# Kernel tuning notes

Measured on AMD Instinct MI355X. Metric: run time of the kernel, lower is better.

Reference implementation:

```python
import jax, jax.numpy as jnp
import numpy as np

B, S, H = 1, 2048, 1024
NH, HD = 16, 64          # num heads, head dim (H = NH*HD)
NT = 1024                # param token num (qkv_slot_num = proj_slot_num)


def pattention(x, key_tokens, value_tokens):
    """Pattention with gelu_l2_norm: x:[...,H] -> [...,out]."""
    attn = jnp.einsum('bsh,th->bst', x, key_tokens)          # scale_factor = 1
    g = jax.nn.gelu(attn, approximate=False)                 # torch F.gelu exact
    norm = jnp.linalg.norm(g, axis=-1, keepdims=True)
    w = g / norm * jnp.sqrt(jnp.asarray(g.shape[-1], g.dtype))
    return jnp.einsum('bst,td->bsd', w, value_tokens)


def setup_inputs() -> dict:
    key = jax.random.key(0)
    ks = jax.random.split(key, 9)
    names = ['q_key', 'q_val', 'k_key', 'k_val', 'v_key', 'v_val', 'proj_key', 'proj_val']
    inp = {'x': jax.random.normal(ks[0], (B, S, H), jnp.float32)}
    for i, n in enumerate(names):
        inp[n] = jax.random.normal(ks[i + 1], (NT, H), jnp.float32) * 0.02
    return inp


def reference(x, q_key, q_val, k_key, k_val, v_key, v_val, proj_key, proj_val):
    # Q/K/V via Pattention (token-parameter attention)
    q = pattention(x, q_key, q_val).reshape(B, S, NH, HD)
    k = pattention(x, k_key, k_val).reshape(B, S, NH, HD)
    v = pattention(x, v_key, v_val).reshape(B, S, NH, HD)
    # causal softmax attention, scale = 1/sqrt(head_dim) (flash default)
    scale = 1.0 / jnp.sqrt(jnp.asarray(HD, q.dtype))
    scores = jnp.einsum('bqhd,bkhd->bhqk', q, k) * scale
    causal = jnp.tril(jnp.ones((S, S), dtype=bool))
    scores = jnp.where(causal, scores, jnp.asarray(-1e30, scores.dtype))
    probs = jax.nn.softmax(scores, axis=-1)
    ctx = jnp.einsum('bhqk,bkhd->bqhd', probs, v).reshape(B, S, H)
    # output projection via Pattention
    return pattention(ctx, proj_key, proj_val)
```

## Files before the change

kernel.cpp:

```cpp
#include <hip/hip_runtime.h>
#include <cstdint>
#include <cstddef>

#define S_LEN 2048
#define H_DIM 1024
#define NTOK  1024
#define NHEAD 16
#define HDIM  64
#define NSPLIT 4

typedef __bf16 bf16;
typedef __bf16 bf16x8 __attribute__((ext_vector_type(8)));
typedef __bf16 bf16x4 __attribute__((ext_vector_type(4)));
typedef float  f32x4  __attribute__((ext_vector_type(4)));

#define QSCALE_LOG2E 0.18033688011112042f

static __device__ __forceinline__ f32x4 mfma16(bf16x8 a, bf16x8 b, f32x4 c) {
    return __builtin_amdgcn_mfma_f32_16x16x32_bf16(a, b, c, 0, 0, 0);
}

static __device__ __forceinline__ void async16(const void* gp, void* lp) {
    __builtin_amdgcn_global_load_lds(
        (const __attribute__((address_space(1))) void*)gp,
        (__attribute__((address_space(3))) void*)lp, 16, 0, 0);
}

static __device__ __forceinline__ float fexp2(float x) {
    return __builtin_amdgcn_exp2f(x);
}

struct PrepArgs {
    const float* csrc[6];
    bf16* cdst[6];
    const float* tsrc[4];
    bf16* tdst[4];
    float* ssq;
};
__global__ __launch_bounds__(256) void prep_kernel(PrepArgs a) {
    __shared__ float t[32][33];
    if (blockIdx.y < 6) {
        if (blockIdx.y == 0 && blockIdx.x == 0) {
#pragma unroll
            for (int i = 0; i < 24; ++i) a.ssq[threadIdx.x + i * 256] = 0.0f;
        }
        const float* __restrict__ s = a.csrc[blockIdx.y];
        bf16* __restrict__ d = a.cdst[blockIdx.y];
        size_t i = ((size_t)blockIdx.x * 256 + threadIdx.x) * 4;
        f32x4 v = *(const f32x4*)&s[i];
        bf16x4 o;
        o[0] = (bf16)v[0]; o[1] = (bf16)v[1]; o[2] = (bf16)v[2]; o[3] = (bf16)v[3];
        *(bf16x4*)&d[i] = o;
    } else {
        const int z = blockIdx.y - 6;
        const float* __restrict__ in = a.tsrc[z];
        bf16* __restrict__ out = a.tdst[z];
        const int bx = (blockIdx.x & 31) * 32, by = (blockIdx.x >> 5) * 32;
        const int x = threadIdx.x & 31, y0 = threadIdx.x >> 5;
#pragma unroll
        for (int j = 0; j < 32; j += 8)
            t[y0 + j][x] = in[(size_t)(by + y0 + j) * 1024 + bx + x];
        __syncthreads();
#pragma unroll
        for (int j = 0; j < 32; j += 8)
            out[(size_t)(bx + y0 + j) * 1024 + by + x] = (bf16)t[x][y0 + j];
    }
}

template <int MODE, typename OutT>
struct GemmArgs {
    const bf16* A[3];
    const bf16* B[3];
    OutT* C[3];
    float* S[3];
    bf16* Ct[3];
    float emul[3];
};

template <int MODE, typename OutT>
__global__ __launch_bounds__(256, 3) void gemm_bt(GemmArgs<MODE, OutT> args) {
    constexpr int Kd = 1024, Nd = 1024, BK = 64;
    const bf16* __restrict__ A = args.A[blockIdx.z];
    const bf16* __restrict__ B = args.B[blockIdx.z];
    OutT* __restrict__ C = args.C[blockIdx.z];
    float* __restrict__ S = args.S[blockIdx.z];
    bf16* __restrict__ Ct = args.Ct[blockIdx.z];
    const float emul = args.emul[blockIdx.z];

    __shared__ __align__(16) bf16 As[2][128 * BK];
    __shared__ __align__(16) bf16 Bs[2][64 * BK];

    const int tid = threadIdx.x;
    const int w = tid >> 6, lane = tid & 63, quad = lane >> 4, m16 = lane & 15;
    const int wm = (w >> 1) * 64, wn = (w & 1) * 32;
    const int bm = blockIdx.y * 128, bn = blockIdx.x * 64;

    const int srow = lane >> 3;
    const int sseg = ((lane & 7) ^ srow) * 8;

    auto stage = [&](int buf, int k0) {
        const bf16* Ab = A + (size_t)bm * Kd + k0;
#pragma unroll
        for (int c = 0; c < 4; ++c) {
            int chunk = w * 4 + c;
            async16(Ab + (size_t)(chunk * 8 + srow) * Kd + sseg,
                    &As[buf][chunk * 512]);
        }
        const bf16* Bb = B + (size_t)bn * Kd + k0;
#pragma unroll
        for (int c = 0; c < 2; ++c) {
            int chunk = w * 2 + c;
            async16(Bb + (size_t)(chunk * 8 + srow) * Kd + sseg,
                    &Bs[buf][chunk * 512]);
        }
    };

    f32x4 acc[4][2] = {};
    stage(0, 0);

    for (int k0 = 0; k0 < Kd; k0 += BK) {
        const int buf = (k0 >> 6) & 1;
        asm volatile("s_waitcnt vmcnt(0)" ::: "memory");
        __syncthreads();
        if (k0 + BK < Kd) stage(buf ^ 1, k0 + BK);

        bf16x8 a[2][4], b[2][2];
#pragma unroll
        for (int kc = 0; kc < 2; ++kc) {
#pragma unroll
            for (int i = 0; i < 4; ++i) {
                int row = wm + i * 16 + m16;
                a[kc][i] = *(const bf16x8*)
                    &As[buf][row * 64 + (((kc * 4 + quad) ^ (row & 7)) << 3)];
            }
#pragma unroll
            for (int j = 0; j < 2; ++j) {
                int row = wn + j * 16 + m16;
                b[kc][j] = *(const bf16x8*)
                    &Bs[buf][row * 64 + (((kc * 4 + quad) ^ (row & 7)) << 3)];
            }
        }
#pragma unroll
        for (int kc = 0; kc < 2; ++kc)
#pragma unroll
            for (int i = 0; i < 4; ++i)
#pragma unroll
                for (int j = 0; j < 2; ++j)
                    acc[i][j] = mfma16(a[kc][i], b[kc][j], acc[i][j]);
    }

    if (MODE == 1) {
        float sq[4][4] = {};
#pragma unroll
        for (int i = 0; i < 4; ++i)
#pragma unroll
            for (int j = 0; j < 2; ++j)
#pragma unroll
                for (int r = 0; r < 4; ++r) {
                    int row = bm + wm + i * 16 + quad * 4 + r;
                    int col = bn + wn + j * 16 + m16;
                    float v = acc[i][j][r];
                    v = 0.5f * v * (1.0f + erff(v * 0.70710678118654752f));
                    C[(size_t)row * Nd + col] = (OutT)v;
                    sq[i][r] += v * v;
                }
#pragma unroll
        for (int i = 0; i < 4; ++i)
#pragma unroll
            for (int r = 0; r < 4; ++r) {
                float s2 = sq[i][r];
                s2 += __shfl_xor(s2, 1);
                s2 += __shfl_xor(s2, 2);
                s2 += __shfl_xor(s2, 4);
                s2 += __shfl_xor(s2, 8);
                if (m16 == 0)
                    atomicAdd(&S[bm + wm + i * 16 + quad * 4 + r], s2);
            }
        return;
    }

    float scl[4][4];
#pragma unroll
    for (int i = 0; i < 4; ++i)
#pragma unroll
        for (int r = 0; r < 4; ++r)
            scl[i][r] =
                32.0f * rsqrtf(S[bm + wm + i * 16 + quad * 4 + r]) * emul;

    if (Ct != nullptr) {
#pragma unroll
        for (int i = 0; i < 4; ++i)
#pragma unroll
            for (int j = 0; j < 2; ++j) {
                int k = bm + wm + i * 16 + quad * 4;
                int col = bn + wn + j * 16 + m16;
                bf16x4 o4;
#pragma unroll
                for (int r = 0; r < 4; ++r)
                    o4[r] = (bf16)(acc[i][j][r] * scl[i][r]);
                int kb = k >> 6, c = (k >> 3) & 7, off = k & 7;
                int pos = ((c ^ (col & 7)) << 3) + off;
                *(bf16x4*)&Ct[(size_t)col * 2048 + kb * 64 + pos] = o4;
            }
        return;
    }

#pragma unroll
    for (int i = 0; i < 4; ++i)
#pragma unroll
        for (int j = 0; j < 2; ++j)
#pragma unroll
            for (int r = 0; r < 4; ++r) {
                int row = bm + wm + i * 16 + quad * 4 + r;
                int col = bn + wn + j * 16 + m16;
                C[(size_t)row * Nd + col] = (OutT)(acc[i][j][r] * scl[i][r]);
            }
}

template <int MODE, typename OutT>
__global__ __launch_bounds__(512) void gemm_bt512(GemmArgs<MODE, OutT> args) {
    constexpr int Kd = 1024, Nd = 1024, BK = 64;
    const bf16* __restrict__ A = args.A[blockIdx.z];
    const bf16* __restrict__ B = args.B[blockIdx.z];
    OutT* __restrict__ C = args.C[blockIdx.z];
    float* __restrict__ S = args.S[blockIdx.z];
    const float emul = args.emul[blockIdx.z];

    __shared__ __align__(16) bf16 As[2][128 * BK];
    __shared__ __align__(16) bf16 Bs[2][64 * BK];

    const int tid = threadIdx.x;
    const int w = tid >> 6, lane = tid & 63, quad = lane >> 4, m16 = lane & 15;
    const int wm = (w >> 1) * 32, wn = (w & 1) * 32;
    const int bm = blockIdx.y * 128, bn = blockIdx.x * 64;

    const int srow = lane >> 3;
    const int sseg = ((lane & 7) ^ srow) * 8;

    auto stage = [&](int buf, int k0) {
        const bf16* Ab = A + (size_t)bm * Kd + k0;
#pragma unroll
        for (int c = 0; c < 2; ++c) {
            int chunk = w * 2 + c;
            async16(Ab + (size_t)(chunk * 8 + srow) * Kd + sseg,
                    &As[buf][chunk * 512]);
        }
        const bf16* Bb = B + (size_t)bn * Kd + k0;
        {
            int chunk = w;
            async16(Bb + (size_t)(chunk * 8 + srow) * Kd + sseg,
                    &Bs[buf][chunk * 512]);
        }
    };

    f32x4 acc[2][2] = {};
    stage(0, 0);

    for (int k0 = 0; k0 < Kd; k0 += BK) {
        const int buf = (k0 >> 6) & 1;
        asm volatile("s_waitcnt vmcnt(0)" ::: "memory");
        __syncthreads();
        if (k0 + BK < Kd) stage(buf ^ 1, k0 + BK);

        bf16x8 a[2][2], b[2][2];
#pragma unroll
        for (int kc = 0; kc < 2; ++kc) {
#pragma unroll
            for (int i = 0; i < 2; ++i) {
                int row = wm + i * 16 + m16;
                a[kc][i] = *(const bf16x8*)
                    &As[buf][row * 64 + (((kc * 4 + quad) ^ (row & 7)) << 3)];
            }
#pragma unroll
            for (int j = 0; j < 2; ++j) {
                int row = wn + j * 16 + m16;
                b[kc][j] = *(const bf16x8*)
                    &Bs[buf][row * 64 + (((kc * 4 + quad) ^ (row & 7)) << 3)];
            }
        }
#pragma unroll
        for (int kc = 0; kc < 2; ++kc)
#pragma unroll
            for (int i = 0; i < 2; ++i)
#pragma unroll
                for (int j = 0; j < 2; ++j)
                    acc[i][j] = mfma16(a[kc][i], b[kc][j], acc[i][j]);
    }

    if (MODE == 1) {
        float sq[2][4] = {};
#pragma unroll
        for (int i = 0; i < 2; ++i)
#pragma unroll
            for (int j = 0; j < 2; ++j)
#pragma unroll
                for (int r = 0; r < 4; ++r) {
                    int row = bm + wm + i * 16 + quad * 4 + r;
                    int col = bn + wn + j * 16 + m16;
                    float v = acc[i][j][r];
                    v = 0.5f * v * (1.0f + erff(v * 0.70710678118654752f));
                    C[(size_t)row * Nd + col] = (OutT)v;
                    sq[i][r] += v * v;
                }
#pragma unroll
        for (int i = 0; i < 2; ++i)
#pragma unroll
            for (int r = 0; r < 4; ++r) {
                float s2 = sq[i][r];
                s2 += __shfl_xor(s2, 1);
                s2 += __shfl_xor(s2, 2);
                s2 += __shfl_xor(s2, 4);
                s2 += __shfl_xor(s2, 8);
                if (m16 == 0)
                    atomicAdd(&S[bm + wm + i * 16 + quad * 4 + r], s2);
            }
        return;
    }

    float scl[2][4];
#pragma unroll
    for (int i = 0; i < 2; ++i)
#pragma unroll
        for (int r = 0; r < 4; ++r)
            scl[i][r] =
                32.0f * rsqrtf(S[bm + wm + i * 16 + quad * 4 + r]) * emul;

#pragma unroll
    for (int i = 0; i < 2; ++i)
#pragma unroll
        for (int j = 0; j < 2; ++j)
#pragma unroll
            for (int r = 0; r < 4; ++r) {
                int row = bm + wm + i * 16 + quad * 4 + r;
                int col = bn + wn + j * 16 + m16;
                C[(size_t)row * Nd + col] = (OutT)(acc[i][j][r] * scl[i][r]);
            }
}

struct FlashArgs {
    const bf16* Q;
    const bf16* K;
    const bf16* VtG;
    bf16* op[NSPLIT];
    float* ml;
};

__global__ __launch_bounds__(256, 3) void flash_kernel(FlashArgs fa) {
    const int bid = blockIdx.x;
    const int h = (bid & 7) * 2 + ((bid >> 3) & 1);
    const int s = (bid >> 4) & 3;
    const int qt = 31 - (bid >> 6);
    const int tid = threadIdx.x;
    const int w = tid >> 6, lane = tid & 63, quad = lane >> 4, m16 = lane & 15;
    const int hOff = h * HDIM;

    __shared__ __align__(16) bf16 Ks[2][64 * 64];
    __shared__ __align__(16) bf16 Vs[2][64 * 64];
    __shared__ __align__(16) bf16 Pw[4][16][72];

    const bf16* VtH = fa.VtG + (size_t)hOff * 2048;
    bf16* __restrict__ Opart = fa.op[s];

    const int trow = tid >> 3, tseg8 = (tid & 7) * 8;

    auto stage = [&](int buf, int k0) {
#pragma unroll
        for (int c = 0; c < 2; ++c) {
            int row = c * 32 + trow;
            int seg = (((tid & 7) ^ (row & 7)) << 3);
            async16(fa.K + (size_t)(k0 + row) * H_DIM + hOff + seg,
                    &Ks[buf][row * 64 + tseg8]);
        }
#pragma unroll
        for (int p = 0; p < 2; ++p) {
            int d = trow + p * 32;
            async16(VtH + (size_t)d * 2048 + k0 + tseg8,
                    &Vs[buf][d * 64 + tseg8]);
        }
    };

    const int qRow = qt * 64 + w * 16 + m16;
    bf16x8 bq[2];
    bq[0] = *(const bf16x8*)&fa.Q[(size_t)qRow * H_DIM + hOff + quad * 8];
    bq[1] = *(const bf16x8*)&fa.Q[(size_t)qRow * H_DIM + hOff + 32 + quad * 8];

    f32x4 oacc[4] = {};
    float m_i = -1e30f, l_i = 0.0f;

    const int cnt = (qt >= s) ? ((qt - s) >> 2) + 1 : 0;
    if (cnt > 0) {
        stage(0, s * 64);
        asm volatile("s_waitcnt vmcnt(0)" ::: "memory");
        __builtin_amdgcn_s_barrier();
    }
    for (int i = 0; i < cnt; ++i) {
        const int kt = s + i * NSPLIT;
        const int k0 = kt * 64;
        const int cur = i & 1;
        const bool diag = (kt == qt);
        if (i + 1 < cnt) stage(cur ^ 1, (kt + NSPLIT) * 64);
        f32x4 sacc[4] = {};
        __builtin_amdgcn_s_setprio(1);
#pragma unroll
        for (int ks = 0; ks < 2; ++ks)
#pragma unroll
            for (int j = 0; j < 4; ++j) {
                int row = j * 16 + m16;
                bf16x8 ak = *(const bf16x8*)
                    &Ks[cur][row * 64 + (((ks * 4 + quad) ^ (row & 7)) << 3)];
                sacc[j] = mfma16(ak, bq[ks], sacc[j]);
            }
        __builtin_amdgcn_s_setprio(0);
        if (diag) {
#pragma unroll
            for (int j = 0; j < 4; ++j)
#pragma unroll
                for (int rr = 0; rr < 4; ++rr) {
                    int kcol = k0 + j * 16 + quad * 4 + rr;
                    if (kcol > qRow) sacc[j][rr] = -1e30f;
                }
        }
        float tj[4];
#pragma unroll
        for (int j = 0; j < 4; ++j)
            tj[j] = fmaxf(fmaxf(sacc[j][0], sacc[j][1]),
                          fmaxf(sacc[j][2], sacc[j][3]));
        float mx = fmaxf(fmaxf(tj[0], tj[1]), fmaxf(tj[2], tj[3]));
        mx = fmaxf(mx, __shfl_xor(mx, 16));
        mx = fmaxf(mx, __shfl_xor(mx, 32));
        if (!__all(mx - m_i <= 11.5f)) {
            float mnew = fmaxf(m_i, mx);
            float alpha = fexp2(m_i - mnew);
            l_i *= alpha;
#pragma unroll
            for (int jd = 0; jd < 4; ++jd)
#pragma unroll
                for (int rr = 0; rr < 4; ++rr) oacc[jd][rr] *= alpha;
            m_i = mnew;
        }
        float lsj[4];
#pragma unroll
        for (int j = 0; j < 4; ++j) {
            bf16x4 pk;
            float p0 = fexp2(sacc[j][0] - m_i);
            float p1 = fexp2(sacc[j][1] - m_i);
            float p2 = fexp2(sacc[j][2] - m_i);
            float p3 = fexp2(sacc[j][3] - m_i);
            pk[0] = (bf16)p0; pk[1] = (bf16)p1;
            pk[2] = (bf16)p2; pk[3] = (bf16)p3;
            lsj[j] = (p0 + p1) + (p2 + p3);
            *(bf16x4*)&Pw[w][m16][j * 16 + quad * 4] = pk;
        }
        float ls = (lsj[0] + lsj[1]) + (lsj[2] + lsj[3]);
        ls += __shfl_xor(ls, 16);
        ls += __shfl_xor(ls, 32);
        l_i += ls;
        __builtin_amdgcn_s_setprio(1);
#pragma unroll
        for (int ks = 0; ks < 2; ++ks) {
            bf16x8 bp = *(const bf16x8*)&Pw[w][m16][ks * 32 + quad * 8];
#pragma unroll
            for (int jd = 0; jd < 4; ++jd) {
                int d = jd * 16 + m16;
                bf16x8 av = *(const bf16x8*)
                    &Vs[cur][d * 64 + (((ks * 4 + quad) ^ (d & 7)) << 3)];
                oacc[jd] = mfma16(av, bp, oacc[jd]);
            }
        }
        __builtin_amdgcn_s_setprio(0);
        asm volatile("s_waitcnt vmcnt(0)" ::: "memory");
        __builtin_amdgcn_s_barrier();
    }
#pragma unroll
    for (int jd = 0; jd < 4; ++jd) {
        bf16x4 o4;
#pragma unroll
        for (int rr = 0; rr < 4; ++rr) o4[rr] = (bf16)oacc[jd][rr];
        *(bf16x4*)&Opart[(size_t)qRow * 1024 + hOff + jd * 16 + quad * 4] = o4;
    }
    if (quad == 0) {
        float* p = fa.ml + ((size_t)(s * 2048 + qRow) * 16 + h) * 2;
        p[0] = m_i;
        p[1] = l_i;
    }
}

struct CombArgs {
    const bf16* op[NSPLIT];
    const float* ml;
    bf16* ctx;
    float* ssp;
};
__global__ __launch_bounds__(256) void combine_kernel(CombArgs ca) {
    if (blockIdx.x < 8) ca.ssp[blockIdx.x * 256 + threadIdx.x] = 0.0f;
    const int unit = blockIdx.x * 4 + (threadIdx.x >> 6);
    const int row = unit >> 4, h = unit & 15;
    const int d = threadIdx.x & 63;
    float mv[NSPLIT], lv[NSPLIT], M = -1e30f;
#pragma unroll
    for (int s2 = 0; s2 < NSPLIT; ++s2) {
        const float* p = ca.ml + ((size_t)(s2 * 2048 + row) * 16 + h) * 2;
        mv[s2] = p[0];
        lv[s2] = p[1];
        M = fmaxf(M, mv[s2]);
    }
    float num = 0.0f, den = 0.0f;
#pragma unroll
    for (int s2 = 0; s2 < NSPLIT; ++s2) {
        float e = fexp2(mv[s2] - M);
        den += lv[s2] * e;
        num += e * (float)ca.op[s2][(size_t)row * 1024 + h * 64 + d];
    }
    ca.ctx[(size_t)row * 1024 + h * 64 + d] = (bf16)(num / den);
}

extern "C" void kernel_launch(void* const* d_in, const int* in_sizes, int n_in,
                              void* d_out, int out_size, void* d_ws,
                              size_t ws_size, hipStream_t stream) {
    const float* x = (const float*)d_in[0];
    const float* keysF[4] = {(const float*)d_in[1], (const float*)d_in[3],
                             (const float*)d_in[5], (const float*)d_in[7]};
    const float* valsF[4] = {(const float*)d_in[2], (const float*)d_in[4],
                             (const float*)d_in[6], (const float*)d_in[8]};
    float* out = (float*)d_out;

    char* ws = (char*)d_ws;
    bf16* xb = (bf16*)(ws);
    bf16* g3[3];
    for (int i = 0; i < 3; ++i) g3[i] = (bf16*)(ws + (4ull << 20) + (size_t)i * (4ull << 20));
    bf16* kb16[4], *vT16[4];
    for (int i = 0; i < 4; ++i) {
        kb16[i] = (bf16*)(ws + (16ull << 20) + (size_t)i * (2ull << 20));
        vT16[i] = (bf16*)(ws + (24ull << 20) + (size_t)i * (2ull << 20));
    }
    bf16* qb    = (bf16*)(ws);
    bf16* kbuf  = (bf16*)(ws + (32ull << 20));
    float* mlbuf = (float*)(ws + (20ull << 20));
    bf16* VtG   = (bf16*)(ws + (36ull << 20));
    bf16* ctx   = (bf16*)(ws + (32ull << 20));
    bf16* projg = (bf16*)(ws + (4ull << 20));

    float* SSq = (float*)d_out;
    float* SSp = (float*)(ws + (21ull << 20));

    bf16* opart[NSPLIT];
    for (int i = 0; i < NSPLIT; ++i)
        opart[i] = (bf16*)(ws + (4ull << 20) + (size_t)i * (4ull << 20));

    PrepArgs pa;
    pa.csrc[0] = x;             pa.cdst[0] = xb;
    pa.csrc[1] = x + (1 << 20); pa.cdst[1] = xb + (1 << 20);
    for (int i = 0; i < 4; ++i) { pa.csrc[2 + i] = keysF[i]; pa.cdst[2 + i] = kb16[i]; }
    for (int i = 0; i < 4; ++i) { pa.tsrc[i] = valsF[i]; pa.tdst[i] = vT16[i]; }
    pa.ssq = SSq;
    prep_kernel<<<dim3(1024, 10), 256, 0, stream>>>(pa);

    GemmArgs<1, bf16> g1;
    for (int z = 0; z < 3; ++z) {
        g1.A[z] = xb; g1.B[z] = kb16[z]; g1.C[z] = g3[z];
        g1.S[z] = SSq + z * 2048; g1.Ct[z] = nullptr; g1.emul[z] = 1.0f;
    }
    gemm_bt<1, bf16><<<dim3(16, 16, 3), 256, 0, stream>>>(g1);

    GemmArgs<2, bf16> g2;
    bf16* qkv[3] = {qb, kbuf, qb };
    for (int z = 0; z < 3; ++z) {
        g2.A[z] = g3[z]; g2.B[z] = vT16[z]; g2.C[z] = qkv[z];
        g2.S[z] = SSq + z * 2048;
        g2.Ct[z] = (z == 2) ? VtG : nullptr;
        g2.emul[z] = (z == 0) ? QSCALE_LOG2E : 1.0f;
    }
    gemm_bt<2, bf16><<<dim3(16, 16, 3), 256, 0, stream>>>(g2);

    FlashArgs fla;
    fla.Q = qb; fla.K = kbuf; fla.VtG = VtG; fla.ml = mlbuf;
    for (int i = 0; i < NSPLIT; ++i) fla.op[i] = opart[i];
    flash_kernel<<<dim3(2048), 256, 0, stream>>>(fla);

    CombArgs cba;
    for (int i = 0; i < NSPLIT; ++i) cba.op[i] = opart[i];
    cba.ml = mlbuf; cba.ctx = ctx; cba.ssp = SSp;
    combine_kernel<<<dim3(8192), 256, 0, stream>>>(cba);

    GemmArgs<1, bf16> p1;
    for (int z = 0; z < 3; ++z) {
        p1.A[z] = ctx; p1.B[z] = kb16[3]; p1.C[z] = projg;
        p1.S[z] = SSp; p1.Ct[z] = nullptr; p1.emul[z] = 1.0f;
    }
    gemm_bt512<1, bf16><<<dim3(16, 16, 1), 512, 0, stream>>>(p1);

    GemmArgs<2, float> p2;
    for (int z = 0; z < 3; ++z) {
        p2.A[z] = projg; p2.B[z] = vT16[3]; p2.C[z] = out;
        p2.S[z] = SSp; p2.Ct[z] = nullptr; p2.emul[z] = 1.0f;
    }
    gemm_bt512<2, float><<<dim3(16, 16, 1), 512, 0, stream>>>(p2);
}
```

Baseline: 212.3 us.

## Halve flash split count, retile projection GEMMs to 64x64, widen prep transpose

Reduces the flash attention KV split from 4 to 2, which halves the grid and the partial outputs the combine kernel must merge. The projection GEMMs move from 512-thread 128x64 tiles to 256-thread 64x64 tiles with twice as many blocks, trading per-block reuse for more parallelism. The prep transpose switches to 64x64 tiles with vector float4 loads and bf16x2 stores. A drain-and-barrier macro replaces the separate waitcnt and barrier calls. Fewer flash blocks may leave CUs less evenly loaded, and the smaller tiles lower operand reuse.

```diff
diff --git a/kernel.cpp b/kernel.cpp
--- a/kernel.cpp
+++ b/kernel.cpp
@@ -7,11 +7,12 @@
 #define NTOK  1024
 #define NHEAD 16
 #define HDIM  64
-#define NSPLIT 4
+#define NSPLIT 2
 
 typedef __bf16 bf16;
 typedef __bf16 bf16x8 __attribute__((ext_vector_type(8)));
 typedef __bf16 bf16x4 __attribute__((ext_vector_type(4)));
+typedef __bf16 bf16x2 __attribute__((ext_vector_type(2)));
 typedef float  f32x4  __attribute__((ext_vector_type(4)));
 
 #define QSCALE_LOG2E 0.18033688011112042f
@@ -29,6 +30,9 @@
 static __device__ __forceinline__ float fexp2(float x) {
     return __builtin_amdgcn_exp2f(x);
 }
+
+#define DRAIN_BARRIER() \
+    asm volatile("s_waitcnt vmcnt(0)\n\ts_barrier" ::: "memory")
 
 struct PrepArgs {
     const float* csrc[6];
@@ -38,7 +42,7 @@
     float* ssq;
 };
 __global__ __launch_bounds__(256) void prep_kernel(PrepArgs a) {
-    __shared__ float t[32][33];
+    __shared__ float t[64][65];
     if (blockIdx.y < 6) {
         if (blockIdx.y == 0 && blockIdx.x == 0) {
 #pragma unroll
@@ -52,18 +56,28 @@
         o[0] = (bf16)v[0]; o[1] = (bf16)v[1]; o[2] = (bf16)v[2]; o[3] = (bf16)v[3];
         *(bf16x4*)&d[i] = o;
     } else {
+        if (blockIdx.x >= 256) return;
         const int z = blockIdx.y - 6;
         const float* __restrict__ in = a.tsrc[z];
         bf16* __restrict__ out = a.tdst[z];
-        const int bx = (blockIdx.x & 31) * 32, by = (blockIdx.x >> 5) * 32;
-        const int x = threadIdx.x & 31, y0 = threadIdx.x >> 5;
-#pragma unroll
-        for (int j = 0; j < 32; j += 8)
-            t[y0 + j][x] = in[(size_t)(by + y0 + j) * 1024 + bx + x];
+        const int bx = (blockIdx.x & 15) * 64, by = (blockIdx.x >> 4) * 64;
+        const int c4 = (threadIdx.x & 15) * 4, r0 = threadIdx.x >> 4;
+#pragma unroll
+        for (int rr = 0; rr < 64; rr += 16) {
+            f32x4 v = *(const f32x4*)&in[(size_t)(by + r0 + rr) * 1024 + bx + c4];
+#pragma unroll
+            for (int j = 0; j < 4; ++j) t[c4 + j][r0 + rr] = v[j];
+        }
         __syncthreads();
-#pragma unroll
-        for (int j = 0; j < 32; j += 8)
-            out[(size_t)(bx + y0 + j) * 1024 + by + x] = (bf16)t[x][y0 + j];
+        const int l2 = (threadIdx.x & 31) * 2, w8 = threadIdx.x >> 5;
+#pragma unroll
+        for (int rr = 0; rr < 64; rr += 8) {
+            int r = w8 + rr;
+            bf16x2 o;
+            o[0] = (bf16)t[r][l2];
+            o[1] = (bf16)t[r][l2 + 1];
+            *(bf16x2*)&out[(size_t)(bx + r) * 1024 + by + l2] = o;
+        }
     }
 }
 
@@ -120,8 +134,7 @@
 
     for (int k0 = 0; k0 < Kd; k0 += BK) {
         const int buf = (k0 >> 6) & 1;
-        asm volatile("s_waitcnt vmcnt(0)" ::: "memory");
-        __syncthreads();
+        DRAIN_BARRIER();
         if (k0 + BK < Kd) stage(buf ^ 1, k0 + BK);
 
         bf16x8 a[2][4], b[2][2];
@@ -218,7 +231,7 @@
 }
 
 template <int MODE, typename OutT>
-__global__ __launch_bounds__(512) void gemm_bt512(GemmArgs<MODE, OutT> args) {
+__global__ __launch_bounds__(256, 2) void gemm_bt64(GemmArgs<MODE, OutT> args) {
     constexpr int Kd = 1024, Nd = 1024, BK = 64;
     const bf16* __restrict__ A = args.A[blockIdx.z];
     const bf16* __restrict__ B = args.B[blockIdx.z];
@@ -226,30 +239,24 @@
     float* __restrict__ S = args.S[blockIdx.z];
     const float emul = args.emul[blockIdx.z];
 
-    __shared__ __align__(16) bf16 As[2][128 * BK];
-    __shared__ __align__(16) bf16 Bs[2][64 * BK];
+    __shared__ __align__(16) bf16 As[2][64 * 64];
+    __shared__ __align__(16) bf16 Bs[2][64 * 64];
 
     const int tid = threadIdx.x;
     const int w = tid >> 6, lane = tid & 63, quad = lane >> 4, m16 = lane & 15;
     const int wm = (w >> 1) * 32, wn = (w & 1) * 32;
-    const int bm = blockIdx.y * 128, bn = blockIdx.x * 64;
-
-    const int srow = lane >> 3;
-    const int sseg = ((lane & 7) ^ srow) * 8;
+    const int bm = blockIdx.y * 64, bn = blockIdx.x * 64;
+    const int trow = tid >> 3, t8 = (tid & 7) * 8;
 
     auto stage = [&](int buf, int k0) {
-        const bf16* Ab = A + (size_t)bm * Kd + k0;
 #pragma unroll
         for (int c = 0; c < 2; ++c) {
-            int chunk = w * 2 + c;
-            async16(Ab + (size_t)(chunk * 8 + srow) * Kd + sseg,
-                    &As[buf][chunk * 512]);
-        }
-        const bf16* Bb = B + (size_t)bn * Kd + k0;
-        {
-            int chunk = w;
-            async16(Bb + (size_t)(chunk * 8 + srow) * Kd + sseg,
-                    &Bs[buf][chunk * 512]);
+            int row = c * 32 + trow;
+            int seg = (((tid & 7) ^ (row & 7)) << 3);
+            async16(A + (size_t)(bm + row) * Kd + k0 + seg,
+                    &As[buf][row * 64 + t8]);
+            async16(B + (size_t)(bn + row) * Kd + k0 + seg,
+                    &Bs[buf][row * 64 + t8]);
         }
     };
 
@@ -258,8 +265,7 @@
 
     for (int k0 = 0; k0 < Kd; k0 += BK) {
         const int buf = (k0 >> 6) & 1;
-        asm volatile("s_waitcnt vmcnt(0)" ::: "memory");
-        __syncthreads();
+        DRAIN_BARRIER();
         if (k0 + BK < Kd) stage(buf ^ 1, k0 + BK);
 
         bf16x8 a[2][2], b[2][2];
@@ -348,8 +354,8 @@
 __global__ __launch_bounds__(256, 3) void flash_kernel(FlashArgs fa) {
     const int bid = blockIdx.x;
     const int h = (bid & 7) * 2 + ((bid >> 3) & 1);
-    const int s = (bid >> 4) & 3;
-    const int qt = 31 - (bid >> 6);
+    const int s = (bid >> 4) & 1;
+    const int qt = 31 - (bid >> 5);
     const int tid = threadIdx.x;
     const int w = tid >> 6, lane = tid & 63, quad = lane >> 4, m16 = lane & 15;
     const int hOff = h * HDIM;
@@ -387,11 +393,10 @@
     f32x4 oacc[4] = {};
     float m_i = -1e30f, l_i = 0.0f;
 
-    const int cnt = (qt >= s) ? ((qt - s) >> 2) + 1 : 0;
+    const int cnt = (qt >= s) ? ((qt - s) >> 1) + 1 : 0;
     if (cnt > 0) {
         stage(0, s * 64);
-        asm volatile("s_waitcnt vmcnt(0)" ::: "memory");
-        __builtin_amdgcn_s_barrier();
+        DRAIN_BARRIER();
     }
     for (int i = 0; i < cnt; ++i) {
         const int kt = s + i * NSPLIT;
@@ -468,8 +473,7 @@
             }
         }
         __builtin_amdgcn_s_setprio(0);
-        asm volatile("s_waitcnt vmcnt(0)" ::: "memory");
-        __builtin_amdgcn_s_barrier();
+        DRAIN_BARRIER();
     }
 #pragma unroll
     for (int jd = 0; jd < 4; ++jd) {
@@ -575,7 +579,7 @@
     FlashArgs fla;
     fla.Q = qb; fla.K = kbuf; fla.VtG = VtG; fla.ml = mlbuf;
     for (int i = 0; i < NSPLIT; ++i) fla.op[i] = opart[i];
-    flash_kernel<<<dim3(2048), 256, 0, stream>>>(fla);
+    flash_kernel<<<dim3(1024), 256, 0, stream>>>(fla);
 
     CombArgs cba;
     for (int i = 0; i < NSPLIT; ++i) cba.op[i] = opart[i];
@@ -587,12 +591,12 @@
         p1.A[z] = ctx; p1.B[z] = kb16[3]; p1.C[z] = projg;
         p1.S[z] = SSp; p1.Ct[z] = nullptr; p1.emul[z] = 1.0f;
     }
-    gemm_bt512<1, bf16><<<dim3(16, 16, 1), 512, 0, stream>>>(p1);
+    gemm_bt64<1, bf16><<<dim3(16, 32, 1), 256, 0, stream>>>(p1);
 
     GemmArgs<2, float> p2;
     for (int z = 0; z < 3; ++z) {
         p2.A[z] = projg; p2.B[z] = vT16[3]; p2.C[z] = out;
         p2.S[z] = SSp; p2.Ct[z] = nullptr; p2.emul[z] = 1.0f;
     }
-    gemm_bt512<2, float><<<dim3(16, 16, 1), 512, 0, stream>>>(p2);
-}
+    gemm_bt64<2, float><<<dim3(16, 32, 1), 256, 0, stream>>>(p2);
+}
```

Measured after the change: 208.3 us (median of 3 runs). Within noise of the previous version (-1.9%).
